# Kernel optimization log

Measured on AMD Instinct MI355X. Metric: run time of the kernel, lower is better.

The kernel has to match this reference:

```python
import jax, jax.numpy as jnp
import numpy as np
from jax import lax


def _box_filter(x, r):
    # depthwise (groups=ch) 2D box conv matching torch nf.conv2d(..., groups=ch)
    ch = x.shape[1]
    k = 2 * r + 1
    kernel = jnp.full((ch, 1, k, k), 1.0 / (k * k), dtype=x.dtype)
    return lax.conv_general_dilated(
        x, kernel,
        window_strides=(1, 1),
        padding=[(r, r), (r, r)],
        feature_group_count=ch,
        dimension_numbers=("NCHW", "OIHW", "NCHW"))


def setup_inputs() -> dict:
    key = jax.random.key(0)
    kx, ky = jax.random.split(key)
    B, C, H, W = 8, 3, 512, 512
    x = jax.random.uniform(kx, (B, C, H, W), dtype=jnp.float32)
    y = jax.random.uniform(ky, (B, C, H, W), dtype=jnp.float32)
    return {"x": x, "y": y, "r": 5}


def reference(x, y, r):
    eps = 0.01
    b, c, h, w = x.shape
    N = _box_filter(jnp.ones((1, 1, h, w), dtype=x.dtype), r)  # [1,1,H,W]
    mean_x = _box_filter(x, r) / N
    mean_y = _box_filter(y, r) / N
    cov_xy = _box_filter(x * y, r) / N - mean_x * mean_y
    var_x = _box_filter(x * x, r) / N - mean_x * mean_x
    A = cov_xy / (var_x + eps)
    bb = mean_y - A * mean_x
    mean_A = _box_filter(A, r) / N
    mean_b = _box_filter(bb, r) / N
    return mean_A * x + mean_b
```

## Files before the change

kernel.cpp:

```cpp
#include <hip/hip_runtime.h>


#define R    5
#define KS   11
#define TX   64
#define TY   16
#define WLO  (TX + 2 * R)
#define PCOLS 94
#define IMG  512

#define P(c) ((c) + ((c) >> 2))

__device__ __forceinline__ int clampcnt(int g) {
    int lo = max(g - R, 0);
    int hi = min(g + R, IMG - 1);
    return hi - lo + 1;
}

__global__ __launch_bounds__(256) void guided_stage_a(
        const float* __restrict__ x, const float* __restrict__ y,
        float2* __restrict__ ab) {
    __shared__ float4 v4[TY][PCOLS];

    const int plane = blockIdx.z;
    const int tx0 = blockIdx.x * TX;
    const int ty0 = blockIdx.y * TY;
    const int tid = threadIdx.x;
    const size_t pbase = (size_t)plane * IMG * IMG;
    const float* xp = x + pbase;
    const float* yp = y + pbase;
    const bool interior = (blockIdx.x > 0) & (blockIdx.x < gridDim.x - 1) &
                          (blockIdx.y > 0) & (blockIdx.y < gridDim.y - 1);

    if (tid < 2 * WLO) {
        const int seg = (tid >= WLO) ? 1 : 0;
        const int cc  = tid - seg * WLO;
        const int r0  = seg * 8;
        const int gx  = tx0 + cc - R;
        const int gy0 = ty0 + r0 - R;

        float xv[18], yv[18];
        if (interior) {
#pragma unroll
            for (int j = 0; j < 18; ++j) {
                size_t o = (size_t)(gy0 + j) * IMG + gx;
                xv[j] = xp[o];
                yv[j] = yp[o];
            }
        } else {
            const bool xok = (gx >= 0 && gx < IMG);
#pragma unroll
            for (int j = 0; j < 18; ++j) {
                int gy = gy0 + j;
                bool ok = xok && ((unsigned)gy < (unsigned)IMG);
                size_t o = (size_t)gy * IMG + gx;
                xv[j] = ok ? xp[o] : 0.f;
                yv[j] = ok ? yp[o] : 0.f;
            }
        }

        float sx = 0.f, sy = 0.f, sxy = 0.f, sxx = 0.f;
#pragma unroll
        for (int j = 0; j < KS; ++j) {
            sx += xv[j]; sy += yv[j];
            sxy += xv[j] * yv[j]; sxx += xv[j] * xv[j];
        }
        v4[r0][P(cc)] = make_float4(sx, sy, sxy, sxx);
#pragma unroll
        for (int s = 1; s < 8; ++s) {
            float xn = xv[s + 10], yn = yv[s + 10];
            float xo = xv[s - 1],  yo = yv[s - 1];
            sx  += xn - xo;
            sy  += yn - yo;
            sxy += xn * yn - xo * yo;
            sxx += xn * xn - xo * xo;
            v4[r0 + s][P(cc)] = make_float4(sx, sy, sxy, sxx);
        }
    }
    __syncthreads();

    {
        const int oy = tid >> 4;
        const int ch = tid & 15;
        const int c0 = ch * 4;
        const int gy = ty0 + oy;

        float sx = 0.f, sy = 0.f, sxy = 0.f, sxx = 0.f;
#pragma unroll
        for (int d = 0; d < KS; ++d) {
            float4 v = v4[oy][P(c0 + d)];
            sx += v.x; sy += v.y; sxy += v.z; sxx += v.w;
        }
        const float cy = (float)clampcnt(gy);
        float2 res[4];
#pragma unroll
        for (int i = 0; i < 4; ++i) {
            const int ox = c0 + i;
            if (i > 0) {
                float4 a = v4[oy][P(ox + 10)];
                float4 b = v4[oy][P(ox - 1)];
                sx += a.x - b.x; sy += a.y - b.y;
                sxy += a.z - b.z; sxx += a.w - b.w;
            }
            float inv = interior ? (1.0f / 121.0f)
                                 : 1.0f / (cy * (float)clampcnt(tx0 + ox));
            float mx = sx * inv, my = sy * inv;
            float cov = sxy * inv - mx * my;
            float var = sxx * inv - mx * mx;
            float A = cov / (var + 0.01f);
            res[i] = make_float2(A, my - A * mx);
        }
        float4* dst = reinterpret_cast<float4*>(&ab[pbase + (size_t)gy * IMG + tx0 + c0]);
        dst[0] = make_float4(res[0].x, res[0].y, res[1].x, res[1].y);
        dst[1] = make_float4(res[2].x, res[2].y, res[3].x, res[3].y);
    }
}

__global__ __launch_bounds__(256) void guided_stage_b(
        const float2* __restrict__ ab, const float* __restrict__ x,
        float* __restrict__ out) {
    __shared__ float2 v2[TY][PCOLS];

    const int plane = blockIdx.z;
    const int tx0 = blockIdx.x * TX;
    const int ty0 = blockIdx.y * TY;
    const int tid = threadIdx.x;
    const size_t pbase = (size_t)plane * IMG * IMG;
    const float2* abp = ab + pbase;
    const float* xp = x + pbase;
    const bool interior = (blockIdx.x > 0) & (blockIdx.x < gridDim.x - 1) &
                          (blockIdx.y > 0) & (blockIdx.y < gridDim.y - 1);

    if (tid < 2 * WLO) {
        const int seg = (tid >= WLO) ? 1 : 0;
        const int cc  = tid - seg * WLO;
        const int r0  = seg * 8;
        const int gx  = tx0 + cc - R;
        const int gy0 = ty0 + r0 - R;

        float2 av[18];
        if (interior) {
#pragma unroll
            for (int j = 0; j < 18; ++j) {
                av[j] = abp[(size_t)(gy0 + j) * IMG + gx];
            }
        } else {
            const bool xok = (gx >= 0 && gx < IMG);
#pragma unroll
            for (int j = 0; j < 18; ++j) {
                int gy = gy0 + j;
                bool ok = xok && ((unsigned)gy < (unsigned)IMG);
                size_t o = (size_t)gy * IMG + gx;
                av[j] = ok ? abp[o] : make_float2(0.f, 0.f);
            }
        }

        float sa = 0.f, sb = 0.f;
#pragma unroll
        for (int j = 0; j < KS; ++j) { sa += av[j].x; sb += av[j].y; }
        v2[r0][P(cc)] = make_float2(sa, sb);
#pragma unroll
        for (int s = 1; s < 8; ++s) {
            sa += av[s + 10].x - av[s - 1].x;
            sb += av[s + 10].y - av[s - 1].y;
            v2[r0 + s][P(cc)] = make_float2(sa, sb);
        }
    }
    __syncthreads();

    {
        const int oy = tid >> 4;
        const int ch = tid & 15;
        const int c0 = ch * 4;
        const int gy = ty0 + oy;

        float sa = 0.f, sb = 0.f;
#pragma unroll
        for (int d = 0; d < KS; ++d) {
            float2 v = v2[oy][P(c0 + d)];
            sa += v.x; sb += v.y;
        }
        const float cy = (float)clampcnt(gy);
        const size_t obase = (size_t)gy * IMG + tx0 + c0;
        const float4 xv4 = *reinterpret_cast<const float4*>(&xp[obase]);
        const float xv[4] = {xv4.x, xv4.y, xv4.z, xv4.w};
        float res[4];
#pragma unroll
        for (int i = 0; i < 4; ++i) {
            const int ox = c0 + i;
            if (i > 0) {
                float2 a = v2[oy][P(ox + 10)];
                float2 b = v2[oy][P(ox - 1)];
                sa += a.x - b.x; sb += a.y - b.y;
            }
            float inv = interior ? (1.0f / 121.0f)
                                 : 1.0f / (cy * (float)clampcnt(tx0 + ox));
            res[i] = (sa * inv) * xv[i] + (sb * inv);
        }
        *reinterpret_cast<float4*>(&out[pbase + obase]) =
            make_float4(res[0], res[1], res[2], res[3]);
    }
}

extern "C" void kernel_launch(void* const* d_in, const int* in_sizes, int n_in,
                              void* d_out, int out_size, void* d_ws, size_t ws_size,
                              hipStream_t stream) {
    const float* x = (const float*)d_in[0];
    const float* y = (const float*)d_in[1];
    float* out = (float*)d_out;
    float2* ab = (float2*)d_ws;

    const int planes = in_sizes[0] / (IMG * IMG);

    dim3 grid(IMG / TX, IMG / TY, planes);
    guided_stage_a<<<grid, 256, 0, stream>>>(x, y, ab);
    guided_stage_b<<<grid, 256, 0, stream>>>(ab, x, out);
}
```

Baseline: 125.9 us.

## Fuse both guided-filter stages into one kernel with halo recompute in LDS

```diff
diff --git a/kernel.cpp b/kernel.cpp
--- a/kernel.cpp
+++ b/kernel.cpp
@@ -2,25 +2,36 @@
 
 
 #define R    5
-#define KS   11
 #define TX   64
 #define TY   16
-#define WLO  (TX + 2 * R)
-#define PCOLS 94
 #define IMG  512
-
-#define P(c) ((c) + ((c) >> 2))
-
-__device__ __forceinline__ int clampcnt(int g) {
-    int lo = max(g - R, 0);
-    int hi = min(g + R, IMG - 1);
-    return hi - lo + 1;
+#define AROWS 26
+#define ACOLS 74
+#define XCOLS 84
+#define PC1  105
+#define QC   84
+#define XSP  68
+
+#define OFF_AB 43680
+#define OFF_XS (OFF_AB + 26*QC*8)
+#define SMEM_TOTAL (OFF_XS + TY*XSP*4)
+
+#define P1(c) ((c) + ((c) >> 2))
+#define Q(c)  ((c) + ((c) >> 3))
+
+__device__ __forceinline__ float ccnt(int g) {
+    int lo = max(g - R, 0), hi = min(g + R, IMG - 1);
+    return (float)(hi - lo + 1);
 }
 
-__global__ __launch_bounds__(256) void guided_stage_a(
+__global__ __launch_bounds__(256) void guided_fused(
         const float* __restrict__ x, const float* __restrict__ y,
-        float2* __restrict__ ab) {
-    __shared__ float4 v4[TY][PCOLS];
+        float* __restrict__ out) {
+    __shared__ __align__(16) unsigned char smem[SMEM_TOTAL];
+    float4 (*v4)[PC1] = (float4(*)[PC1])smem;
+    float2 (*ab2)[QC] = (float2(*)[QC])(smem + OFF_AB);
+    float2 (*vab)[QC] = (float2(*)[QC])smem;
+    float  (*xs)[XSP] = (float(*)[XSP])(smem + OFF_XS);
 
     const int plane = blockIdx.z;
     const int tx0 = blockIdx.x * TX;
@@ -32,25 +43,26 @@
     const bool interior = (blockIdx.x > 0) & (blockIdx.x < gridDim.x - 1) &
                           (blockIdx.y > 0) & (blockIdx.y < gridDim.y - 1);
 
-    if (tid < 2 * WLO) {
-        const int seg = (tid >= WLO) ? 1 : 0;
-        const int cc  = tid - seg * WLO;
-        const int r0  = seg * 8;
-        const int gx  = tx0 + cc - R;
-        const int gy0 = ty0 + r0 - R;
-
-        float xv[18], yv[18];
+    if (tid < 3 * XCOLS) {
+        const int seg = tid / XCOLS;
+        const int cc  = tid - seg * XCOLS;
+        const int r0  = seg * 9;
+        const int gx  = tx0 - 2 * R + cc;
+        const int gy0 = ty0 - 2 * R + r0;
+
+        float xv[19], yv[19];
         if (interior) {
-#pragma unroll
-            for (int j = 0; j < 18; ++j) {
-                size_t o = (size_t)(gy0 + j) * IMG + gx;
-                xv[j] = xp[o];
-                yv[j] = yp[o];
+            const float* xc = xp + (size_t)gy0 * IMG + gx;
+            const float* yc = yp + (size_t)gy0 * IMG + gx;
+#pragma unroll
+            for (int j = 0; j < 19; ++j) {
+                xv[j] = xc[(size_t)j * IMG];
+                yv[j] = yc[(size_t)j * IMG];
             }
         } else {
-            const bool xok = (gx >= 0 && gx < IMG);
-#pragma unroll
-            for (int j = 0; j < 18; ++j) {
+            const bool xok = ((unsigned)gx < (unsigned)IMG);
+#pragma unroll
+            for (int j = 0; j < 19; ++j) {
                 int gy = gy0 + j;
                 bool ok = xok && ((unsigned)gy < (unsigned)IMG);
                 size_t o = (size_t)gy * IMG + gx;
@@ -58,23 +70,88 @@
                 yv[j] = ok ? yp[o] : 0.f;
             }
         }
-
+        if (seg == 1 && cc >= 10 && cc < 10 + TX) {
+#pragma unroll
+            for (int o = 0; o < TY; ++o) xs[o][cc - 10] = xv[o + 1];
+        }
         float sx = 0.f, sy = 0.f, sxy = 0.f, sxx = 0.f;
 #pragma unroll
-        for (int j = 0; j < KS; ++j) {
+        for (int j = 0; j < 11; ++j) {
             sx += xv[j]; sy += yv[j];
             sxy += xv[j] * yv[j]; sxx += xv[j] * xv[j];
         }
-        v4[r0][P(cc)] = make_float4(sx, sy, sxy, sxx);
-#pragma unroll
-        for (int s = 1; s < 8; ++s) {
+        v4[r0][P1(cc)] = make_float4(sx, sy, sxy, sxx);
+#pragma unroll
+        for (int s = 1; s < 9; ++s) {
+            const int r = r0 + s;
             float xn = xv[s + 10], yn = yv[s + 10];
             float xo = xv[s - 1],  yo = yv[s - 1];
             sx  += xn - xo;
             sy  += yn - yo;
             sxy += xn * yn - xo * yo;
             sxx += xn * xn - xo * xo;
-            v4[r0 + s][P(cc)] = make_float4(sx, sy, sxy, sxx);
+            if (r < AROWS) v4[r][P1(cc)] = make_float4(sx, sy, sxy, sxx);
+        }
+    }
+    __syncthreads();
+
+#pragma unroll 1
+    for (int t = tid; t < AROWS * 10; t += 256) {
+        const int r  = t / 10;
+        const int ch = t - r * 10;
+        const int c0 = ch * 8;
+        const int ay = ty0 - R + r;
+        float sx = 0.f, sy = 0.f, sxy = 0.f, sxx = 0.f;
+#pragma unroll
+        for (int d = 0; d < 11; ++d) {
+            float4 v = v4[r][P1(c0 + d)];
+            sx += v.x; sy += v.y; sxy += v.z; sxx += v.w;
+        }
+        const float cy = ccnt(ay);
+#pragma unroll
+        for (int i = 0; i < 8; ++i) {
+            const int ac = c0 + i;
+            if (ac >= ACOLS) break;
+            if (i > 0) {
+                float4 a = v4[r][P1(ac + 10)];
+                float4 b = v4[r][P1(ac - 1)];
+                sx += a.x - b.x; sy += a.y - b.y;
+                sxy += a.z - b.z; sxx += a.w - b.w;
+            }
+            const int ax = tx0 - R + ac;
+            float A = 0.f, bb = 0.f;
+            if (interior || (((unsigned)ay < (unsigned)IMG) &&
+                             ((unsigned)ax < (unsigned)IMG))) {
+                float inv = interior ? (1.0f / 121.0f)
+                                     : 1.0f / (cy * ccnt(ax));
+                float mx = sx * inv, my = sy * inv;
+                float cov = sxy * inv - mx * my;
+                float var = sxx * inv - mx * mx;
+                A = cov / (var + 0.01f);
+                bb = my - A * mx;
+            }
+            ab2[r][Q(ac)] = make_float2(A, bb);
+        }
+    }
+    __syncthreads();
+
+    if (tid < 2 * ACOLS) {
+        const int hseg = (tid >= ACOLS) ? 1 : 0;
+        const int ac = tid - hseg * ACOLS;
+        const int r0 = hseg * 8;
+        float sa = 0.f, sb = 0.f;
+#pragma unroll
+        for (int d = 0; d < 11; ++d) {
+            float2 v = ab2[r0 + d][Q(ac)];
+            sa += v.x; sb += v.y;
+        }
+        vab[r0][Q(ac)] = make_float2(sa, sb);
+#pragma unroll
+        for (int s = 1; s < 8; ++s) {
+            float2 a = ab2[r0 + s + 10][Q(ac)];
+            float2 b = ab2[r0 + s - 1][Q(ac)];
+            sa += a.x - b.x; sb += a.y - b.y;
+            vab[r0 + s][Q(ac)] = make_float2(sa, sb);
         }
     }
     __syncthreads();
@@ -84,120 +161,29 @@
         const int ch = tid & 15;
         const int c0 = ch * 4;
         const int gy = ty0 + oy;
-
-        float sx = 0.f, sy = 0.f, sxy = 0.f, sxx = 0.f;
-#pragma unroll
-        for (int d = 0; d < KS; ++d) {
-            float4 v = v4[oy][P(c0 + d)];
-            sx += v.x; sy += v.y; sxy += v.z; sxx += v.w;
-        }
-        const float cy = (float)clampcnt(gy);
-        float2 res[4];
-#pragma unroll
-        for (int i = 0; i < 4; ++i) {
-            const int ox = c0 + i;
-            if (i > 0) {
-                float4 a = v4[oy][P(ox + 10)];
-                float4 b = v4[oy][P(ox - 1)];
-                sx += a.x - b.x; sy += a.y - b.y;
-                sxy += a.z - b.z; sxx += a.w - b.w;
-            }
-            float inv = interior ? (1.0f / 121.0f)
-                                 : 1.0f / (cy * (float)clampcnt(tx0 + ox));
-            float mx = sx * inv, my = sy * inv;
-            float cov = sxy * inv - mx * my;
-            float var = sxx * inv - mx * mx;
-            float A = cov / (var + 0.01f);
-            res[i] = make_float2(A, my - A * mx);
-        }
-        float4* dst = reinterpret_cast<float4*>(&ab[pbase + (size_t)gy * IMG + tx0 + c0]);
-        dst[0] = make_float4(res[0].x, res[0].y, res[1].x, res[1].y);
-        dst[1] = make_float4(res[2].x, res[2].y, res[3].x, res[3].y);
-    }
-}
-
-__global__ __launch_bounds__(256) void guided_stage_b(
-        const float2* __restrict__ ab, const float* __restrict__ x,
-        float* __restrict__ out) {
-    __shared__ float2 v2[TY][PCOLS];
-
-    const int plane = blockIdx.z;
-    const int tx0 = blockIdx.x * TX;
-    const int ty0 = blockIdx.y * TY;
-    const int tid = threadIdx.x;
-    const size_t pbase = (size_t)plane * IMG * IMG;
-    const float2* abp = ab + pbase;
-    const float* xp = x + pbase;
-    const bool interior = (blockIdx.x > 0) & (blockIdx.x < gridDim.x - 1) &
-                          (blockIdx.y > 0) & (blockIdx.y < gridDim.y - 1);
-
-    if (tid < 2 * WLO) {
-        const int seg = (tid >= WLO) ? 1 : 0;
-        const int cc  = tid - seg * WLO;
-        const int r0  = seg * 8;
-        const int gx  = tx0 + cc - R;
-        const int gy0 = ty0 + r0 - R;
-
-        float2 av[18];
-        if (interior) {
-#pragma unroll
-            for (int j = 0; j < 18; ++j) {
-                av[j] = abp[(size_t)(gy0 + j) * IMG + gx];
-            }
-        } else {
-            const bool xok = (gx >= 0 && gx < IMG);
-#pragma unroll
-            for (int j = 0; j < 18; ++j) {
-                int gy = gy0 + j;
-                bool ok = xok && ((unsigned)gy < (unsigned)IMG);
-                size_t o = (size_t)gy * IMG + gx;
-                av[j] = ok ? abp[o] : make_float2(0.f, 0.f);
-            }
-        }
-
         float sa = 0.f, sb = 0.f;
 #pragma unroll
-        for (int j = 0; j < KS; ++j) { sa += av[j].x; sb += av[j].y; }
-        v2[r0][P(cc)] = make_float2(sa, sb);
-#pragma unroll
-        for (int s = 1; s < 8; ++s) {
-            sa += av[s + 10].x - av[s - 1].x;
-            sb += av[s + 10].y - av[s - 1].y;
-            v2[r0 + s][P(cc)] = make_float2(sa, sb);
-        }
-    }
-    __syncthreads();
-
-    {
-        const int oy = tid >> 4;
-        const int ch = tid & 15;
-        const int c0 = ch * 4;
-        const int gy = ty0 + oy;
-
-        float sa = 0.f, sb = 0.f;
-#pragma unroll
-        for (int d = 0; d < KS; ++d) {
-            float2 v = v2[oy][P(c0 + d)];
+        for (int d = 0; d < 11; ++d) {
+            float2 v = vab[oy][Q(c0 + d)];
             sa += v.x; sb += v.y;
         }
-        const float cy = (float)clampcnt(gy);
-        const size_t obase = (size_t)gy * IMG + tx0 + c0;
-        const float4 xv4 = *reinterpret_cast<const float4*>(&xp[obase]);
+        const float cy = ccnt(gy);
+        const float4 xv4 = *reinterpret_cast<const float4*>(&xs[oy][c0]);
         const float xv[4] = {xv4.x, xv4.y, xv4.z, xv4.w};
         float res[4];
 #pragma unroll
         for (int i = 0; i < 4; ++i) {
-            const int ox = c0 + i;
+            const int l = c0 + i;
             if (i > 0) {
-                float2 a = v2[oy][P(ox + 10)];
-                float2 b = v2[oy][P(ox - 1)];
+                float2 a = vab[oy][Q(l + 10)];
+                float2 b = vab[oy][Q(l - 1)];
                 sa += a.x - b.x; sb += a.y - b.y;
             }
             float inv = interior ? (1.0f / 121.0f)
-                                 : 1.0f / (cy * (float)clampcnt(tx0 + ox));
+                                 : 1.0f / (cy * ccnt(tx0 + l));
             res[i] = (sa * inv) * xv[i] + (sb * inv);
         }
-        *reinterpret_cast<float4*>(&out[pbase + obase]) =
+        *reinterpret_cast<float4*>(&out[pbase + (size_t)gy * IMG + tx0 + c0]) =
             make_float4(res[0], res[1], res[2], res[3]);
     }
 }
@@ -208,11 +194,9 @@
     const float* x = (const float*)d_in[0];
     const float* y = (const float*)d_in[1];
     float* out = (float*)d_out;
-    float2* ab = (float2*)d_ws;
 
     const int planes = in_sizes[0] / (IMG * IMG);
 
     dim3 grid(IMG / TX, IMG / TY, planes);
-    guided_stage_a<<<grid, 256, 0, stream>>>(x, y, ab);
-    guided_stage_b<<<grid, 256, 0, stream>>>(ab, x, out);
+    guided_fused<<<grid, 256, 0, stream>>>(x, y, out);
 }
```

Measured after the change: 160.6 us. 27.5% more time.
